# Kernel optimization log

Hardware: AMD Instinct MI355X
Metric: run time of the kernel (lower is better)

The kernel has to match this reference:

```python
import jax, jax.numpy as jnp
import numpy as np

D_MODEL = 1024
NUM_HEAD = 16
D_HEAD = 64


def setup_inputs() -> dict:
    key = jax.random.key(0)
    ks = jax.random.split(key, 9)
    b, p = 8, 1024
    s = 1.0 / np.sqrt(D_MODEL)
    inp = {
        "x": jax.random.normal(ks[0], (b, p, D_MODEL), jnp.float32),
        "w_q": jax.random.uniform(ks[1], (D_MODEL, D_MODEL), jnp.float32, -s, s),
        "b_q": jax.random.uniform(ks[2], (D_MODEL,), jnp.float32, -s, s),
        "w_k": jax.random.uniform(ks[3], (D_MODEL, D_MODEL), jnp.float32, -s, s),
        "b_k": jax.random.uniform(ks[4], (D_MODEL,), jnp.float32, -s, s),
        "w_v": jax.random.uniform(ks[5], (D_MODEL, D_MODEL), jnp.float32, -s, s),
        "b_v": jax.random.uniform(ks[6], (D_MODEL,), jnp.float32, -s, s),
        "w_o": jax.random.uniform(ks[7], (D_MODEL, D_MODEL), jnp.float32, -s, s),
        "b_o": jax.random.uniform(ks[8], (D_MODEL,), jnp.float32, -s, s),
    }
    return inp


def reference(x, w_q, b_q, w_k, b_k, w_v, b_v, w_o, b_o):
    b, p, _ = x.shape
    # projections (torch Linear: y = x @ W.T + b; here weights stored [in,out])
    q = x @ w_q + b_q
    k = x @ w_k + b_k
    v = x @ w_v + b_v
    # [b, h, p, d]
    q = q.reshape(b, p, NUM_HEAD, D_HEAD).transpose(0, 2, 1, 3)
    k = k.reshape(b, p, NUM_HEAD, D_HEAD).transpose(0, 2, 1, 3)
    v = v.reshape(b, p, NUM_HEAD, D_HEAD).transpose(0, 2, 1, 3)
    scale = 1.0 / np.sqrt(D_HEAD).astype(np.float32)
    scores = jnp.einsum("bhqd,bhkd->bhqk", q, k) * scale
    attn = jax.nn.softmax(scores, axis=-1)
    out = jnp.einsum("bhqk,bhkd->bhqd", attn, v)
    out = out.transpose(0, 2, 1, 3).reshape(b, p, D_MODEL)
    return out @ w_o + b_o
```

## Files before the change

### kernel.cpp

```cpp
#include <hip/hip_runtime.h>
#include <stdint.h>


typedef __attribute__((ext_vector_type(8))) short short8;
typedef __attribute__((ext_vector_type(4))) short s16x4;
typedef __attribute__((ext_vector_type(4))) float f32x4;

__device__ __forceinline__ short f2bf(float f) {
  unsigned u = __builtin_bit_cast(unsigned, f);
  u += 0x7fffu + ((u >> 16) & 1u);
  return (short)(u >> 16);
}

__device__ __forceinline__ unsigned pk2bf(float a, float b) {
  unsigned ua = __builtin_bit_cast(unsigned, a);
  unsigned ub = __builtin_bit_cast(unsigned, b);
  ua += 0x7fffu + ((ua >> 16) & 1u);
  ub += 0x7fffu + ((ub >> 16) & 1u);
  return (ua >> 16) | (ub & 0xffff0000u);
}

__device__ __forceinline__ unsigned cvtpk(float a, float b) {
  unsigned r;
  asm("v_cvt_pk_bf16_f32 %0, %1, %2" : "=v"(r) : "v"(a), "v"(b));
  return r;
}

__device__ __forceinline__ float fexp2(float x) {
  float r;
  asm("v_exp_f32 %0, %1" : "=v"(r) : "v"(x));
  return r;
}

typedef __attribute__((address_space(3))) void lds_void;
typedef __attribute__((address_space(1))) void gbl_void;
#define GLD16(gp, lp) \
  __builtin_amdgcn_global_load_lds((gbl_void*)(gp), (lds_void*)(lp), 16, 0, 0)

#define MFMA(a, b, c) __builtin_amdgcn_mfma_f32_16x16x32_bf16((a), (b), (c), 0, 0, 0)

__global__ __launch_bounds__(256) void k_prep(const float* __restrict__ x,
                                              short* __restrict__ xb,
                                              const float* __restrict__ s0,
                                              const float* __restrict__ s1,
                                              const float* __restrict__ s2,
                                              const float* __restrict__ s3,
                                              short* __restrict__ d0,
                                              short* __restrict__ d1,
                                              short* __restrict__ d2,
                                              short* __restrict__ d3) {
  if (blockIdx.z == 4) {
    int t = threadIdx.y * 32 + threadIdx.x;
    int bid = blockIdx.y * 32 + blockIdx.x;
#pragma unroll
    for (int j = 0; j < 8; ++j) {
      int i = (bid * 2048 + j * 256 + t) * 8;
      const float4* s = (const float4*)(x + i);
      float4 f0 = s[0], f1 = s[1];
      short8 o;
      o[0] = f2bf(f0.x); o[1] = f2bf(f0.y); o[2] = f2bf(f0.z); o[3] = f2bf(f0.w);
      o[4] = f2bf(f1.x); o[5] = f2bf(f1.y); o[6] = f2bf(f1.z); o[7] = f2bf(f1.w);
      *(short8*)(xb + i) = o;
    }
    return;
  }
  __shared__ float tile[64][33];
  const float* srcs[4] = {s0, s1, s2, s3};
  short* dsts[4] = {d0, d1, d2, d3};
  const float* src = srcs[blockIdx.z];
  short* dst = dsts[blockIdx.z];
  int tx = threadIdx.x, ty = threadIdx.y;
  int x0 = blockIdx.x * 32, y0 = blockIdx.y * 64;
#pragma unroll
  for (int i = 0; i < 64; i += 8)
    tile[ty + i][tx] = src[(y0 + ty + i) * 1024 + x0 + tx];
  __syncthreads();
#pragma unroll
  for (int i = 0; i < 32; i += 8) {
    int r = ty + i;
    *(int*)&dst[(x0 + r) * 1024 + y0 + 2 * tx] =
        (int)pk2bf(tile[2 * tx][r], tile[2 * tx + 1][r]);
  }
}

template <int MODE>
__global__ __launch_bounds__(256, 3) void k_gemm(const short* __restrict__ A,
                                                 const short* __restrict__ Bt,
                                                 const float* __restrict__ bias0,
                                                 const float* __restrict__ bias1,
                                                 const float* __restrict__ bias2,
                                                 short* __restrict__ o0,
                                                 short* __restrict__ o1,
                                                 short* __restrict__ o2,
                                                 float* __restrict__ of) {
  __shared__ __align__(16) short a_lds[128 * 64];
  __shared__ __align__(16) short b_lds[128 * 64];
  const int tid = threadIdx.x;
  const int l = blockIdx.x;
  const int m0 = ((((l & 7) << 3) | ((l >> 3) & 7))) << 7;
  const int n0 = (l >> 6) << 7;
  const int w = tid >> 6;
  const int lane = tid & 63;
  const int ll = lane & 15;
  const int qd = lane >> 4;
  const int wm = (w & 1) * 64;
  const int wn = (w >> 1) * 64;

  const int srow = tid >> 3;
  const int schunk = ((tid & 7) ^ (srow & 7)) * 8;
  const short* ag = A + (long)(m0 + srow) * 1024 + schunk;
  const short* bg = Bt + (long)(n0 + srow) * 1024 + schunk;

  f32x4 acc[4][4] = {};

  for (int kt = 0; kt < 1024; kt += 64) {
#pragma unroll
    for (int j = 0; j < 4; ++j) {
      GLD16(ag + j * 32768 + kt, &a_lds[j * 2048 + tid * 8]);
      GLD16(bg + j * 32768 + kt, &b_lds[j * 2048 + tid * 8]);
    }
    __syncthreads();
#pragma unroll
    for (int kh = 0; kh < 2; ++kh) {
      const int xoff = (((kh * 4 + qd) ^ (ll & 7)) * 8);
      short8 af[4], bfr[4];
#pragma unroll
      for (int mt = 0; mt < 4; ++mt)
        af[mt] = *(const short8*)&a_lds[(wm + mt * 16 + ll) * 64 + xoff];
#pragma unroll
      for (int nt = 0; nt < 4; ++nt)
        bfr[nt] = *(const short8*)&b_lds[(wn + nt * 16 + ll) * 64 + xoff];
#pragma unroll
      for (int mt = 0; mt < 4; ++mt)
#pragma unroll
        for (int nt = 0; nt < 4; ++nt)
          acc[mt][nt] = MFMA(af[mt], bfr[nt], acc[mt][nt]);
    }
    __syncthreads();
  }

  if (MODE == 0) {
#pragma unroll
    for (int nt = 0; nt < 4; ++nt) {
      int n = n0 + wn + nt * 16 + ll;
      int which = n >> 10;
      int nl = n & 1023;
      int h = nl >> 6, d = n & 63;
      if (which == 2) {
        float bv = bias2[nl];
        const int b = m0 >> 10;
        const int p0 = (m0 & 1023) + wm;
#pragma unroll
        for (int mt = 0; mt < 4; ++mt) {
          int p = p0 + mt * 16 + qd * 4;
          int2 pk;
          pk.x = (int)pk2bf(acc[mt][nt][0] + bv, acc[mt][nt][1] + bv);
          pk.y = (int)pk2bf(acc[mt][nt][2] + bv, acc[mt][nt][3] + bv);
          *(int2*)&o2[(long)(b * 16 + h) * 65536 + d * 1024 + p] = pk;
        }
      } else {
        float bv = (which == 0) ? bias0[nl] : bias1[nl];
        float sc = (which == 0) ? 0.18033688f : 1.0f;
        short* o = (which == 0) ? o0 : o1;
#pragma unroll
        for (int mt = 0; mt < 4; ++mt) {
#pragma unroll
          for (int r = 0; r < 4; ++r) {
            int m = m0 + wm + mt * 16 + qd * 4 + r;
            int b = m >> 10, p = m & 1023;
            o[(long)(b * 16 + h) * 65536 + p * 64 + d] = f2bf((acc[mt][nt][r] + bv) * sc);
          }
        }
      }
    }
  } else {
#pragma unroll
    for (int nt = 0; nt < 4; ++nt) {
      int n = n0 + wn + nt * 16 + ll;
      float bv = bias0[n];
#pragma unroll
      for (int mt = 0; mt < 4; ++mt) {
#pragma unroll
        for (int r = 0; r < 4; ++r) {
          int m = m0 + wm + mt * 16 + qd * 4 + r;
          of[(long)m * 1024 + n] = acc[mt][nt][r] + bv;
        }
      }
    }
  }
}

__global__ __launch_bounds__(256, 4) void k_attn(const short* __restrict__ Q,
                                                 const short* __restrict__ K,
                                                 const short* __restrict__ VT,
                                                 short* __restrict__ O) {
  __shared__ __align__(16) short k_lds[2][4096];
  __shared__ __align__(16) short vt_lds[2][4096];
  const int tid = threadIdx.x;
  const int w = tid >> 6, lane = tid & 63, ll = lane & 15, qd = lane >> 4;
  const int bid = blockIdx.x;
  const int xcd = bid & 7;
  const int inner = bid >> 3;
  const int bh = xcd * 16 + (inner & 15);
  const int qb = inner >> 4;
  const long hoff = (long)bh * 65536;
  const int qr0 = qb * 128 + w * 32;

  const short* qg = Q + hoff + (long)(qr0 + ll) * 64 + qd * 8;
  short8 qf[2][2];
  qf[0][0] = *(const short8*)qg;
  qf[0][1] = *(const short8*)(qg + 32);
  qf[1][0] = *(const short8*)(qg + 1024);
  qf[1][1] = *(const short8*)(qg + 1024 + 32);

  const int sr = tid >> 3;
  const int swz = (tid & 7) ^ (sr & 7);
  const int pr = (sr & 0x23) | ((sr & 0x0C) << 1) | ((sr & 0x10) >> 2);
  const short* kg = K + hoff + pr * 64 + swz * 8;
  const short* vg = VT + hoff + (long)sr * 1024 + swz * 8;

  const int swzr = ll & 7;
  const int fro0 = ll * 64 + ((qd ^ swzr) * 8);
  const int fro1 = ll * 64 + (((4 + qd) ^ swzr) * 8);

  short8 ones;
#pragma unroll
  for (int i = 0; i < 8; ++i) ones[i] = (short)0x3F80;

  f32x4 oacc[2][4] = {};
  f32x4 lacc[2] = {};

  GLD16(kg, &k_lds[0][tid * 8]);
  GLD16(kg + 2048, &k_lds[0][2048 + tid * 8]);
  GLD16(vg, &vt_lds[0][tid * 8]);
  GLD16(vg + 32768, &vt_lds[0][2048 + tid * 8]);
  __syncthreads();

#pragma unroll 2
  for (int c = 0; c < 16; ++c) {
    const int cur = c & 1, nxt = cur ^ 1;
    if (c < 15) {
      GLD16(kg + (c + 1) * 4096, &k_lds[nxt][tid * 8]);
      GLD16(kg + (c + 1) * 4096 + 2048, &k_lds[nxt][2048 + tid * 8]);
      GLD16(vg + (c + 1) * 64, &vt_lds[nxt][tid * 8]);
      GLD16(vg + (c + 1) * 64 + 32768, &vt_lds[nxt][2048 + tid * 8]);
    }

    f32x4 s[2][4];
    __builtin_amdgcn_s_setprio(1);
#pragma unroll
    for (int jt = 0; jt < 4; ++jt) {
      short8 kf0 = *(const short8*)&k_lds[cur][jt * 1024 + fro0];
      short8 kf1 = *(const short8*)&k_lds[cur][jt * 1024 + fro1];
      f32x4 t0 = {};
      t0 = MFMA(kf0, qf[0][0], t0);
      t0 = MFMA(kf1, qf[0][1], t0);
      s[0][jt] = t0;
      f32x4 t1 = {};
      t1 = MFMA(kf0, qf[1][0], t1);
      t1 = MFMA(kf1, qf[1][1], t1);
      s[1][jt] = t1;
    }
    __builtin_amdgcn_s_setprio(0);

    short8 pf[2][2];
#pragma unroll
    for (int g = 0; g < 2; ++g) {
#pragma unroll
      for (int jt = 0; jt < 4; ++jt)
#pragma unroll
        for (int r = 0; r < 4; ++r)
          s[g][jt][r] = fexp2(s[g][jt][r]);
#pragma unroll
      for (int u = 0; u < 2; ++u) {
        union { short8 v; unsigned x[4]; } pk;
        pk.x[0] = cvtpk(s[g][2 * u][0], s[g][2 * u][1]);
        pk.x[1] = cvtpk(s[g][2 * u][2], s[g][2 * u][3]);
        pk.x[2] = cvtpk(s[g][2 * u + 1][0], s[g][2 * u + 1][1]);
        pk.x[3] = cvtpk(s[g][2 * u + 1][2], s[g][2 * u + 1][3]);
        pf[g][u] = pk.v;
      }
    }

    __builtin_amdgcn_s_setprio(1);
#pragma unroll
    for (int dt = 0; dt < 4; ++dt) {
      short8 vf0 = *(const short8*)&vt_lds[cur][dt * 1024 + fro0];
      short8 vf1 = *(const short8*)&vt_lds[cur][dt * 1024 + fro1];
      oacc[0][dt] = MFMA(vf0, pf[0][0], oacc[0][dt]);
      oacc[0][dt] = MFMA(vf1, pf[0][1], oacc[0][dt]);
      oacc[1][dt] = MFMA(vf0, pf[1][0], oacc[1][dt]);
      oacc[1][dt] = MFMA(vf1, pf[1][1], oacc[1][dt]);
    }
    lacc[0] = MFMA(ones, pf[0][0], lacc[0]);
    lacc[0] = MFMA(ones, pf[0][1], lacc[0]);
    lacc[1] = MFMA(ones, pf[1][0], lacc[1]);
    lacc[1] = MFMA(ones, pf[1][1], lacc[1]);
    __builtin_amdgcn_s_setprio(0);
    __syncthreads();
  }

  const int b = bh >> 4, h = bh & 15;
#pragma unroll
  for (int g = 0; g < 2; ++g) {
    const float inv = 1.0f / lacc[g][0];
    const long row = (long)(b * 1024 + qr0 + g * 16 + ll);
#pragma unroll
    for (int dt = 0; dt < 4; ++dt) {
      int2 ov;
      ov.x = (int)cvtpk(oacc[g][dt][0] * inv, oacc[g][dt][1] * inv);
      ov.y = (int)cvtpk(oacc[g][dt][2] * inv, oacc[g][dt][3] * inv);
      *(int2*)&O[row * 1024 + h * 64 + dt * 16 + qd * 4] = ov;
    }
  }
}

extern "C" void kernel_launch(void* const* d_in, const int* in_sizes, int n_in,
                              void* d_out, int out_size, void* d_ws, size_t ws_size,
                              hipStream_t stream) {
  const float* x   = (const float*)d_in[0];
  const float* w_q = (const float*)d_in[1];
  const float* b_q = (const float*)d_in[2];
  const float* w_k = (const float*)d_in[3];
  const float* b_k = (const float*)d_in[4];
  const float* w_v = (const float*)d_in[5];
  const float* b_v = (const float*)d_in[6];
  const float* w_o = (const float*)d_in[7];
  const float* b_o = (const float*)d_in[8];

  char* ws = (char*)d_ws;
  short* xb    = (short*)(ws);
  short* wqkvT = (short*)(ws + (16ull << 20));
  short* woT   = (short*)(ws + (22ull << 20));
  short* qw    = (short*)(ws + (24ull << 20));
  short* kw    = (short*)(ws + (40ull << 20));
  short* vw    = (short*)(ws + (56ull << 20));

  k_prep<<<dim3(32, 16, 5), dim3(32, 8), 0, stream>>>(
      x, xb, w_q, w_k, w_v, w_o,
      wqkvT, wqkvT + (1 << 20), wqkvT + (2 << 20), woT);

  k_gemm<0><<<1536, 256, 0, stream>>>(xb, wqkvT, b_q, b_k, b_v,
                                      qw, kw, vw, nullptr);

  k_attn<<<dim3(1024), 256, 0, stream>>>(qw, kw, vw, xb);

  k_gemm<1><<<512, 256, 0, stream>>>(xb, woT, b_o, nullptr, nullptr,
                                     nullptr, nullptr, nullptr, (float*)d_out);
}
```

Measured before the change: 219.2 us.

## Fuse all four stages into one persistent cooperative kernel with grid syncs

Replaces the four separate launches (prep, QKV GEMM, attention, output GEMM) with a single cooperative persistent kernel. Each stage loops over virtual block indices, and stages are separated by grid.sync(). The aim is to remove launch gaps and kernel-boundary drains. In exchange, every stage now shares one register and LDS budget, losing the per-kernel launch bounds of 3 or 4 blocks. Occupancy is queried on the host on every call, and the grid syncs may cost more than the launch gaps they replace.

```diff
diff --git a/kernel.cpp b/kernel.cpp
--- a/kernel.cpp
+++ b/kernel.cpp
@@ -1,9 +1,11 @@
 #include <hip/hip_runtime.h>
+#include <hip/hip_cooperative_groups.h>
 #include <stdint.h>
 
+namespace cg = cooperative_groups;
+
 
 typedef __attribute__((ext_vector_type(8))) short short8;
-typedef __attribute__((ext_vector_type(4))) short s16x4;
 typedef __attribute__((ext_vector_type(4))) float f32x4;
 
 __device__ __forceinline__ short f2bf(float f) {
@@ -39,64 +41,20 @@
 
 #define MFMA(a, b, c) __builtin_amdgcn_mfma_f32_16x16x32_bf16((a), (b), (c), 0, 0, 0)
 
-__global__ __launch_bounds__(256) void k_prep(const float* __restrict__ x,
-                                              short* __restrict__ xb,
-                                              const float* __restrict__ s0,
-                                              const float* __restrict__ s1,
-                                              const float* __restrict__ s2,
-                                              const float* __restrict__ s3,
-                                              short* __restrict__ d0,
-                                              short* __restrict__ d1,
-                                              short* __restrict__ d2,
-                                              short* __restrict__ d3) {
-  if (blockIdx.z == 4) {
-    int t = threadIdx.y * 32 + threadIdx.x;
-    int bid = blockIdx.y * 32 + blockIdx.x;
-#pragma unroll
-    for (int j = 0; j < 8; ++j) {
-      int i = (bid * 2048 + j * 256 + t) * 8;
-      const float4* s = (const float4*)(x + i);
-      float4 f0 = s[0], f1 = s[1];
-      short8 o;
-      o[0] = f2bf(f0.x); o[1] = f2bf(f0.y); o[2] = f2bf(f0.z); o[3] = f2bf(f0.w);
-      o[4] = f2bf(f1.x); o[5] = f2bf(f1.y); o[6] = f2bf(f1.z); o[7] = f2bf(f1.w);
-      *(short8*)(xb + i) = o;
-    }
-    return;
-  }
-  __shared__ float tile[64][33];
-  const float* srcs[4] = {s0, s1, s2, s3};
-  short* dsts[4] = {d0, d1, d2, d3};
-  const float* src = srcs[blockIdx.z];
-  short* dst = dsts[blockIdx.z];
-  int tx = threadIdx.x, ty = threadIdx.y;
-  int x0 = blockIdx.x * 32, y0 = blockIdx.y * 64;
-#pragma unroll
-  for (int i = 0; i < 64; i += 8)
-    tile[ty + i][tx] = src[(y0 + ty + i) * 1024 + x0 + tx];
-  __syncthreads();
-#pragma unroll
-  for (int i = 0; i < 32; i += 8) {
-    int r = ty + i;
-    *(int*)&dst[(x0 + r) * 1024 + y0 + 2 * tx] =
-        (int)pk2bf(tile[2 * tx][r], tile[2 * tx + 1][r]);
-  }
-}
-
 template <int MODE>
-__global__ __launch_bounds__(256, 3) void k_gemm(const short* __restrict__ A,
-                                                 const short* __restrict__ Bt,
-                                                 const float* __restrict__ bias0,
-                                                 const float* __restrict__ bias1,
-                                                 const float* __restrict__ bias2,
-                                                 short* __restrict__ o0,
-                                                 short* __restrict__ o1,
-                                                 short* __restrict__ o2,
-                                                 float* __restrict__ of) {
-  __shared__ __align__(16) short a_lds[128 * 64];
-  __shared__ __align__(16) short b_lds[128 * 64];
+__device__ __forceinline__ void gemm_tile(int l, char* smem,
+                                          const short* __restrict__ A,
+                                          const short* __restrict__ Bt,
+                                          const float* __restrict__ bias0,
+                                          const float* __restrict__ bias1,
+                                          const float* __restrict__ bias2,
+                                          short* __restrict__ o0,
+                                          short* __restrict__ o1,
+                                          short* __restrict__ o2,
+                                          float* __restrict__ of) {
+  short* a_lds = (short*)smem;
+  short* b_lds = (short*)(smem + 16384);
   const int tid = threadIdx.x;
-  const int l = blockIdx.x;
   const int m0 = ((((l & 7) << 3) | ((l >> 3) & 7))) << 7;
   const int n0 = (l >> 6) << 7;
   const int w = tid >> 6;
@@ -190,15 +148,15 @@
   }
 }
 
-__global__ __launch_bounds__(256, 4) void k_attn(const short* __restrict__ Q,
-                                                 const short* __restrict__ K,
-                                                 const short* __restrict__ VT,
-                                                 short* __restrict__ O) {
-  __shared__ __align__(16) short k_lds[2][4096];
-  __shared__ __align__(16) short vt_lds[2][4096];
+__device__ __forceinline__ void attn_block(int bid, char* smem,
+                                           const short* __restrict__ Q,
+                                           const short* __restrict__ K,
+                                           const short* __restrict__ VT,
+                                           short* __restrict__ O) {
+  short (*k_lds)[4096] = (short (*)[4096])smem;
+  short (*vt_lds)[4096] = (short (*)[4096])(smem + 16384);
   const int tid = threadIdx.x;
   const int w = tid >> 6, lane = tid & 63, ll = lane & 15, qd = lane >> 4;
-  const int bid = blockIdx.x;
   const int xcd = bid & 7;
   const int inner = bid >> 3;
   const int bh = xcd * 16 + (inner & 15);
@@ -313,6 +271,75 @@
       *(int2*)&O[row * 1024 + h * 64 + dt * 16 + qd * 4] = ov;
     }
   }
+}
+
+__global__ __launch_bounds__(256, 4) void k_fused(
+    const float* __restrict__ x,
+    const float* __restrict__ w_q, const float* __restrict__ w_k,
+    const float* __restrict__ w_v, const float* __restrict__ w_o,
+    const float* __restrict__ b_q, const float* __restrict__ b_k,
+    const float* __restrict__ b_v, const float* __restrict__ b_o,
+    short* __restrict__ xb, short* __restrict__ wqkvT, short* __restrict__ woT,
+    short* __restrict__ qw, short* __restrict__ kw, short* __restrict__ vw,
+    float* __restrict__ out) {
+  cg::grid_group grid = cg::this_grid();
+  __shared__ __align__(16) char smem[32768];
+  const int tid = threadIdx.x;
+  const int nb = gridDim.x;
+
+  for (int vb = blockIdx.x; vb < 2560; vb += nb) {
+    const int vbz = vb >> 9;
+    if (vbz == 4) {
+      int bid = vb & 511;
+#pragma unroll
+      for (int j = 0; j < 8; ++j) {
+        int i = (bid * 2048 + j * 256 + tid) * 8;
+        const float4* s = (const float4*)(x + i);
+        float4 f0 = s[0], f1 = s[1];
+        short8 o;
+        o[0] = f2bf(f0.x); o[1] = f2bf(f0.y); o[2] = f2bf(f0.z); o[3] = f2bf(f0.w);
+        o[4] = f2bf(f1.x); o[5] = f2bf(f1.y); o[6] = f2bf(f1.z); o[7] = f2bf(f1.w);
+        *(short8*)(xb + i) = o;
+      }
+    } else {
+      const float* srcs[4] = {w_q, w_k, w_v, w_o};
+      short* dsts[4] = {wqkvT, wqkvT + (1 << 20), wqkvT + (2 << 20), woT};
+      const float* src = srcs[vbz];
+      short* dst = dsts[vbz];
+      float (*tile)[33] = (float (*)[33])smem;
+      int tx = tid & 31, ty = tid >> 5;
+      int u = vb & 511;
+      int x0 = (u & 31) * 32, y0 = (u >> 5) * 64;
+#pragma unroll
+      for (int i = 0; i < 64; i += 8)
+        tile[ty + i][tx] = src[(y0 + ty + i) * 1024 + x0 + tx];
+      __syncthreads();
+#pragma unroll
+      for (int i = 0; i < 32; i += 8) {
+        int r = ty + i;
+        *(int*)&dst[(x0 + r) * 1024 + y0 + 2 * tx] =
+            (int)pk2bf(tile[2 * tx][r], tile[2 * tx + 1][r]);
+      }
+      __syncthreads();
+    }
+  }
+
+  grid.sync();
+
+  for (int vb = blockIdx.x; vb < 1536; vb += nb)
+    gemm_tile<0>(vb, smem, xb, wqkvT, b_q, b_k, b_v, qw, kw, vw, nullptr);
+
+  grid.sync();
+
+  for (int vb = blockIdx.x; vb < 1024; vb += nb) {
+    attn_block(vb, smem, qw, kw, vw, xb);
+    __syncthreads();
+  }
+
+  grid.sync();
+
+  for (int vb = blockIdx.x; vb < 512; vb += nb)
+    gemm_tile<1>(vb, smem, xb, woT, b_o, nullptr, nullptr, nullptr, nullptr, nullptr, out);
 }
 
 extern "C" void kernel_launch(void* const* d_in, const int* in_sizes, int n_in,
@@ -327,6 +354,7 @@
   const float* b_v = (const float*)d_in[6];
   const float* w_o = (const float*)d_in[7];
   const float* b_o = (const float*)d_in[8];
+  float* out = (float*)d_out;
 
   char* ws = (char*)d_ws;
   short* xb    = (short*)(ws);
@@ -336,15 +364,16 @@
   short* kw    = (short*)(ws + (40ull << 20));
   short* vw    = (short*)(ws + (56ull << 20));
 
-  k_prep<<<dim3(32, 16, 5), dim3(32, 8), 0, stream>>>(
-      x, xb, w_q, w_k, w_v, w_o,
-      wqkvT, wqkvT + (1 << 20), wqkvT + (2 << 20), woT);
-
-  k_gemm<0><<<1536, 256, 0, stream>>>(xb, wqkvT, b_q, b_k, b_v,
-                                      qw, kw, vw, nullptr);
-
-  k_attn<<<dim3(1024), 256, 0, stream>>>(qw, kw, vw, xb);
-
-  k_gemm<1><<<512, 256, 0, stream>>>(xb, woT, b_o, nullptr, nullptr,
-                                     nullptr, nullptr, nullptr, (float*)d_out);
-}
+  int maxB = 0;
+  hipOccupancyMaxActiveBlocksPerMultiprocessor(&maxB, k_fused, 256, 0);
+  int gridBlocks = (maxB > 0) ? (maxB * 256) : 768;
+  if (gridBlocks > 1024) gridBlocks = 1024;
+
+  void* args[] = {
+      (void*)&x,  (void*)&w_q, (void*)&w_k, (void*)&w_v, (void*)&w_o,
+      (void*)&b_q, (void*)&b_k, (void*)&b_v, (void*)&b_o,
+      (void*)&xb, (void*)&wqkvT, (void*)&woT,
+      (void*)&qw, (void*)&kw, (void*)&vw, (void*)&out};
+
+  hipLaunchCooperativeKernel(k_fused, dim3(gridBlocks), dim3(256), args, 0, stream);
+}
```

Result: slower. 456.2 us (+108.1%).
